# Kernel optimization log

Measured on AMD Instinct MI355X. Metric: run time of the kernel, lower is better.

## Reference

```python
import jax, jax.numpy as jnp
import numpy as np

B, T, D, H, W = 2, 16, 64, 64, 64
E, EXP = 4, 2
TWO_D = 2 * D
HID = EXP * TWO_D


def layernorm(x, g, b, eps=1e-5):
    m = x.mean(-1, keepdims=True)
    v = ((x - m) ** 2).mean(-1, keepdims=True)
    return (x - m) / jnp.sqrt(v + eps) * g + b


def pscan(A, X):
    # h_t = A_t * h_{t-1} + X_t, scanned over axis=1 (time); complex-valued.
    def comb(c1, c2):
        a1, x1 = c1
        a2, x2 = c2
        return a1 * a2, a2 * x1 + x2
    return jax.lax.associative_scan(comb, (A, X), axis=1)[1]


def setup_inputs() -> dict:
    key = jax.random.key(0)
    ks = jax.random.split(key, 24)
    def s(i, shape, scale=0.05):
        return jax.random.normal(ks[i], shape, jnp.float32) * scale
    return {
        "x_re": jax.random.normal(ks[0], (B, T, D, H, W), jnp.float32),
        "x_im": jax.random.normal(ks[1], (B, T, D, H, W), jnp.float32),
        "dt": jax.random.uniform(ks[2], (T,), jnp.float32, 0.5, 1.5),
        "ln_s_g": jnp.ones((TWO_D,), jnp.float32),
        "ln_s_b": jnp.zeros((TWO_D,), jnp.float32),
        "conv_w": s(3, (TWO_D, TWO_D, 3, 3)),
        "conv_b": jnp.zeros((TWO_D,), jnp.float32),
        "ln_t_g": jnp.ones((TWO_D,), jnp.float32),
        "ln_t_b": jnp.zeros((TWO_D,), jnp.float32),
        "enc_re": s(4, (D, D)), "enc_im": s(5, (D, D)),
        "dec_re": s(6, (D, D)), "dec_im": s(7, (D, D)),
        "alpha": s(8, (D,), 0.5), "omega": s(9, (D,), 1.0),
        "wg": s(10, (TWO_D, D)), "bg": jnp.zeros((D,), jnp.float32),
        "p_re": s(11, (D, D)), "p_im": s(12, (D, D)),
        "w_drift": s(13, (TWO_D, D)), "b_drift": jnp.zeros((D,), jnp.float32),
        "w_router": s(14, (TWO_D, E)),
        "w1": s(15, (E, TWO_D, HID)), "w2": s(16, (E, HID, TWO_D)),
        "noise_scale": jnp.float32(0.01),
    }


def reference(x_re, x_im, dt, ln_s_g, ln_s_b, conv_w, conv_b, ln_t_g, ln_t_b,
              enc_re, enc_im, dec_re, dec_im, alpha, omega, wg, bg,
              p_re, p_im, w_drift, b_drift, w_router, w1, w2, noise_scale):
    x = x_re + 1j * x_im  # [B,T,D,H,W] complex64
    N = B * T
    xf = x.reshape(N, D, H, W)
    xr = jnp.concatenate([xf.real, xf.imag], axis=1)  # [N,2D,H,W]
    # spatial LayerNorm over channels
    xn = layernorm(xr.transpose(0, 2, 3, 1), ln_s_g, ln_s_b).transpose(0, 3, 1, 2)
    # Clifford spatial conv (standard 3x3 same-conv on stacked re/im channels)
    xs = jax.lax.conv_general_dilated(xn, conv_w, (1, 1), 'SAME',
                                      dimension_numbers=('NCHW', 'OIHW', 'NCHW'))
    xs = xs + conv_b[None, :, None, None]
    x_sc = xs[:, :D] + 1j * xs[:, D:]            # [N,D,H,W]
    x5 = x_sc.reshape(B, T, D, H, W)              # complex
    # basis encode: complex channel mixing
    enc = enc_re + 1j * enc_im
    u_t = jnp.einsum('bthwd,de->bthwe', x5.transpose(0, 1, 3, 4, 2), enc)  # [B,T,H,W,D]

    # ---- global flux tracker (pscan #1) ----
    x_mean = x5.mean(axis=(-2, -1))               # [B,T,D] complex
    feat = jnp.concatenate([x_mean.real, x_mean.imag], axis=-1)  # [B,T,2D]
    gate = jax.nn.sigmoid(feat @ wg + bg)         # [B,T,D]
    flux_A = gate.astype(jnp.complex64)
    flux_X = (1.0 - gate) * x_mean
    flux_state = pscan(flux_A, flux_X)            # [B,T,D]
    flux_out = flux_state @ (p_re + 1j * p_im)    # [B,T,D]
    drift_in = jnp.concatenate([flux_out.real, flux_out.imag], axis=-1)
    drift = drift_in @ w_drift + b_drift          # [B,T,D] (dead code in source; kept for fidelity)
    drift_c = drift[..., : D // 2] + 1j * drift[..., D // 2:]
    del drift_c

    # ---- temporal propagation (pscan #2) ----
    dt_e = dt.reshape(1, T, 1, 1, 1)              # broadcast (B,T,H,W,1)
    lam = -jax.nn.softplus(alpha) + 1j * omega    # [D]
    decay = jnp.exp(lam * dt_e)                   # [1,T,1,1,D]
    forcing = (decay - 1.0) / lam                 # ZOH forcing operator
    u_scaled = u_t * forcing                      # [B,T,H,W,D]
    decay_full = jnp.broadcast_to(decay, (B, T, H, W, D))
    A_time = decay_full.transpose(0, 2, 3, 1, 4).reshape(B * H * W, T, D)
    X_time = u_scaled.transpose(0, 2, 3, 1, 4).reshape(B * H * W, T, D)
    Y = pscan(A_time, X_time)
    u_out = Y.reshape(B, H, W, T, D).transpose(0, 3, 1, 2, 4)  # [B,T,H,W,D]
    # deterministic surrogate for the SDE stochastic term (state-proportional)
    u_out = u_out + noise_scale * jnp.sqrt(dt_e) * u_out
    dec = dec_re + 1j * dec_im
    x_out = jnp.einsum('bthwd,de->bthwe', u_out, dec)  # decode
    x_out = x_out.transpose(0, 1, 4, 2, 3).reshape(N, D, H, W)
    xo_r = jnp.concatenate([x_out.real, x_out.imag], axis=1)
    xo_n = layernorm(xo_r.transpose(0, 2, 3, 1), ln_t_g, ln_t_b)  # [N,H,W,2D]

    # ---- MoE FFN over pixels (soft mixture of experts) ----
    gates = jax.nn.softmax(xo_n @ w_router, axis=-1)  # [N,H,W,E]
    acc = jnp.zeros_like(xo_n)
    for e in range(E):
        h = jax.nn.gelu(xo_n @ w1[e])
        acc = acc + gates[..., e:e + 1] * (h @ w2[e])
    delta = acc[..., :D] + 1j * acc[..., D:]          # [N,H,W,D]
    delta = delta.transpose(0, 3, 1, 2).reshape(B, T, D, H, W)
    return x + delta
```

## Files before the change

### kernel.cpp

```cpp
#include <hip/hip_runtime.h>
#include <hip/hip_bf16.h>

#define BB 2
#define TT 16
#define DD 64
#define HH 64
#define WW 64
#define NPIX 131072


typedef unsigned short u16;
typedef unsigned int u32;
typedef __attribute__((ext_vector_type(8))) short bf16x8;
typedef __attribute__((ext_vector_type(4))) float f32x4;

union U16x8 { uint4 u4; uint2 u2[2]; u16 h[8]; bf16x8 v; };

__device__ __forceinline__ float us2f(u16 u) {
  union { u32 i; float f; } c; c.i = ((u32)u) << 16; return c.f;
}
__device__ __forceinline__ u16 f2us(float f) {
  u32 x = __float_as_uint(f);
  u32 r = x + 0x7fffu + ((x >> 16) & 1u);
  return (u16)(r >> 16);
}

__global__ __launch_bounds__(256) void k0_prep(
    const float* __restrict__ conv_w,
    const float* __restrict__ enc_re, const float* __restrict__ enc_im,
    const float* __restrict__ dec_re, const float* __restrict__ dec_im,
    const float* __restrict__ w1, const float* __restrict__ w2,
    u16* __restrict__ mencs, u16* __restrict__ mdecs,
    u16* __restrict__ wcs, u16* __restrict__ w1s, u16* __restrict__ w2s) {
  int idx = blockIdx.x * 256 + threadIdx.x;
  if (idx < 65536) {
    int m = idx >> 15;
    int z = idx & 32767;
    int s = z >> 14;
    int q = z & 16383;
    int j = q & 7, lane = (q >> 3) & 63, ks = (q >> 9) & 3, nt = (q >> 11) & 7;
    int k = ks * 32 + (lane >> 4) * 8 + j;
    int n = nt * 16 + (lane & 15);
    const float* mre = m ? dec_re : enc_re;
    const float* mim = m ? dec_im : enc_im;
    float v;
    if (k < 64) v = (n < 64) ?  mre[k * 64 + n]        : mim[k * 64 + n - 64];
    else        v = (n < 64) ? -mim[(k - 64) * 64 + n] : mre[(k - 64) * 64 + n - 64];
    u16 hi = f2us(v);
    u16 val = s ? f2us(v - us2f(hi)) : hi;
    u16* dst = m ? mdecs : mencs;
    dst[((nt * 8 + s * 4 + ks) * 64 + lane) * 8 + j] = val;
  } else if (idx < 212992) {
    int z = idx - 65536;
    int j = z & 7, lane = (z >> 3) & 63, ks = (z >> 9) & 3, nt = (z >> 11) & 7, tap = z >> 14;
    int ic = ks * 32 + (lane >> 4) * 8 + j;
    int oc = nt * 16 + (lane & 15);
    wcs[z] = f2us(conv_w[(oc * 128 + ic) * 9 + tap]);
  } else if (idx < 344064) {
    int z = idx - 212992;
    int j = z & 7, lane = (z >> 3) & 63, ks = (z >> 9) & 3, nt = (z >> 11) & 15, e = z >> 15;
    int k = ks * 32 + (lane >> 4) * 8 + j;
    int nn = nt * 16 + (lane & 15);
    w1s[z] = f2us(w1[e * 32768 + k * 256 + nn]);
  } else if (idx < 475136) {
    int z = idx - 344064;
    int j = z & 7, lane = (z >> 3) & 63, ks = (z >> 9) & 7, nt = (z >> 12) & 7, e = z >> 15;
    int k = ks * 32 + (lane >> 4) * 8 + j;
    int nn = nt * 16 + (lane & 15);
    w2s[z] = f2us(w2[e * 32768 + k * 128 + nn]);
  }
}

__global__ __launch_bounds__(256) void k1_spatial_ln(
    const float* __restrict__ x_re, const float* __restrict__ x_im,
    const float* __restrict__ g, const float* __restrict__ b,
    u16* __restrict__ xn) {
  __shared__ float tile[64 * 129];
  __shared__ float meanA[64], rstdA[64];
  int n = blockIdx.x >> 6, h = blockIdx.x & 63;
  int tid = threadIdx.x;
  for (int k = 0; k < 32; ++k) {
    int flat = tid + k * 256;
    int c = flat >> 6, w = flat & 63;
    float v = (c < 64) ? x_re[n * 262144 + c * 4096 + h * 64 + w]
                       : x_im[n * 262144 + (c - 64) * 4096 + h * 64 + w];
    tile[w * 129 + c] = v;
  }
  __syncthreads();
  int p = tid >> 2, q = tid & 3;
  float s = 0.f, ss = 0.f;
  for (int c = q * 32; c < q * 32 + 32; ++c) {
    float v = tile[p * 129 + c];
    s += v; ss += v * v;
  }
  s += __shfl_xor(s, 1); ss += __shfl_xor(ss, 1);
  s += __shfl_xor(s, 2); ss += __shfl_xor(ss, 2);
  if (q == 0) {
    float m = s * (1.0f / 128.0f);
    float var = ss * (1.0f / 128.0f) - m * m;
    meanA[p] = m; rstdA[p] = rsqrtf(var + 1e-5f);
  }
  __syncthreads();
  int rowbase = (n * 4096 + h * 64) * 128;
  for (int k = 0; k < 32; ++k) {
    int flat = tid + k * 256;
    int pp = flat >> 7, c = flat & 127;
    float v = (tile[pp * 129 + c] - meanA[pp]) * rstdA[pp] * g[c] + b[c];
    xn[rowbase + flat] = f2us(v);
  }
}

__global__ __launch_bounds__(256) void k2_mfma(
    const u16* __restrict__ xn, const u16* __restrict__ wcs,
    const float* __restrict__ conv_b, u16* __restrict__ xs) {
  __shared__ __align__(16) u16 Xs[3 * 66 * 132];
  int tid = threadIdx.x;
  int wave = tid >> 6, lane = tid & 63;
  int quad = lane >> 4, am = lane & 15;
  int n = blockIdx.x >> 6, h = blockIdx.x & 63;

  for (int dh = 0; dh < 3; ++dh) {
    int hs = h + dh - 1;
    bool valid = (hs >= 0) && (hs < 64);
    const u16* src = xn + (n * 4096 + hs * 64) * 128;
    for (int c = 0; c < 4; ++c) {
      int f8 = tid + c * 256;
      int px = f8 >> 4, ch = (f8 & 15) * 8;
      uint2 lo = make_uint2(0, 0), hi = make_uint2(0, 0);
      if (valid) {
        const uint2* s2 = (const uint2*)(src + px * 128 + ch);
        lo = s2[0]; hi = s2[1];
      }
      u16* dst = Xs + (dh * 66 + px + 1) * 132 + ch;
      *(uint2*)dst = lo;
      *(uint2*)(dst + 4) = hi;
    }
  }
  for (int z = tid; z < 792; z += 256) {
    int dh = z / 264, r = z % 264;
    int px = (r < 132) ? 0 : 65;
    Xs[(dh * 66 + px) * 132 + (r % 132)] = 0;
  }
  __syncthreads();

  f32x4 acc[8];
#pragma unroll
  for (int nt = 0; nt < 8; ++nt) {
    float bv = conv_b[nt * 16 + am];
    acc[nt] = (f32x4){bv, bv, bv, bv};
  }
  int mt = wave;
  for (int tap = 0; tap < 9; ++tap) {
    int dh = tap / 3, dw = tap % 3;
    const u16* arow = Xs + (dh * 66 + mt * 16 + am + dw) * 132 + quad * 8;
    bf16x8 a[4];
#pragma unroll
    for (int ks = 0; ks < 4; ++ks) {
      U16x8 t;
      t.u2[0] = *(const uint2*)(arow + ks * 32);
      t.u2[1] = *(const uint2*)(arow + ks * 32 + 4);
      a[ks] = t.v;
    }
    const uint4* wp = (const uint4*)wcs + tap * 2048 + lane;
    uint4 wb[4];
#pragma unroll
    for (int ks = 0; ks < 4; ++ks) wb[ks] = wp[ks * 64];
    for (int nt = 0; nt < 8; ++nt) {
      uint4 wn[4];
      if (nt < 7) {
#pragma unroll
        for (int ks = 0; ks < 4; ++ks) wn[ks] = wp[((nt + 1) * 4 + ks) * 64];
      }
#pragma unroll
      for (int ks = 0; ks < 4; ++ks) {
        U16x8 bf; bf.u4 = wb[ks];
        acc[nt] = __builtin_amdgcn_mfma_f32_16x16x32_bf16(a[ks], bf.v, acc[nt], 0, 0, 0);
      }
      if (nt < 7) {
#pragma unroll
        for (int ks = 0; ks < 4; ++ks) wb[ks] = wn[ks];
      }
    }
  }
  int rowg = n * 4096 + h * 64;
#pragma unroll
  for (int nt = 0; nt < 8; ++nt)
#pragma unroll
    for (int r = 0; r < 4; ++r)
      xs[(rowg + mt * 16 + quad * 4 + r) * 128 + nt * 16 + am] = f2us(acc[nt][r]);
}

__global__ __launch_bounds__(256) void k3_mfma(
    u16* X, const u16* __restrict__ ms) {
  int tid = threadIdx.x;
  int wave = tid >> 6, lane = tid & 63;
  int quad = lane >> 4, am = lane & 15;
  int rowbase = blockIdx.x * 128 + wave * 32;

  bf16x8 ax[2][4];
#pragma unroll
  for (int mt = 0; mt < 2; ++mt) {
    const uint4* ar = (const uint4*)(X + (rowbase + mt * 16 + am) * 128 + quad * 8);
#pragma unroll
    for (int ks = 0; ks < 4; ++ks) { U16x8 t; t.u4 = ar[ks * 4]; ax[mt][ks] = t.v; }
  }
  const uint4* mp = (const uint4*)ms + lane;
  uint4 wb[8];
#pragma unroll
  for (int kk = 0; kk < 8; ++kk) wb[kk] = mp[kk * 64];
  for (int nt = 0; nt < 8; ++nt) {
    uint4 wn[8];
    if (nt < 7) {
#pragma unroll
      for (int kk = 0; kk < 8; ++kk) wn[kk] = mp[((nt + 1) * 8 + kk) * 64];
    }
    f32x4 ca = (f32x4){0.f, 0.f, 0.f, 0.f};
    f32x4 cb = (f32x4){0.f, 0.f, 0.f, 0.f};
#pragma unroll
    for (int kk = 0; kk < 8; ++kk) {
      U16x8 bf; bf.u4 = wb[kk];
      ca = __builtin_amdgcn_mfma_f32_16x16x32_bf16(ax[0][kk & 3], bf.v, ca, 0, 0, 0);
      cb = __builtin_amdgcn_mfma_f32_16x16x32_bf16(ax[1][kk & 3], bf.v, cb, 0, 0, 0);
    }
#pragma unroll
    for (int r = 0; r < 4; ++r) {
      X[(rowbase + quad * 4 + r) * 128 + nt * 16 + am]      = f2us(ca[r]);
      X[(rowbase + 16 + quad * 4 + r) * 128 + nt * 16 + am] = f2us(cb[r]);
    }
    if (nt < 7) {
#pragma unroll
      for (int kk = 0; kk < 8; ++kk) wb[kk] = wn[kk];
    }
  }
}

__global__ __launch_bounds__(256) void k_scan(
    u16* __restrict__ u, const float* __restrict__ dt,
    const float* __restrict__ alpha, const float* __restrict__ omega,
    const float* __restrict__ ns_p) {
  int flat = blockIdx.x * 256 + threadIdx.x;
  int d = flat & 63;
  int hw = (flat >> 6) & 4095;
  int b = flat >> 18;
  float a = alpha[d];
  float sp = (a > 20.f) ? a : log1pf(expf(a));
  float lr = -sp, li = omega[d];
  float inv_l2 = 1.0f / (lr * lr + li * li);
  float ns = ns_p[0];
  float yr = 0.f, yi = 0.f;
  const int stride = 4096 * 128;
  int base0 = b * 16 * stride + hw * 128 + d;
  for (int t = 0; t < 16; ++t) {
    float dtv = dt[t];
    float er = expf(lr * dtv);
    float ang = li * dtv;
    float dr = er * cosf(ang), di = er * sinf(ang);
    float fr = ((dr - 1.f) * lr + di * li) * inv_l2;
    float fi = (di * lr - (dr - 1.f) * li) * inv_l2;
    int idx = base0 + t * stride;
    float ur = us2f(u[idx]), ui = us2f(u[idx + 64]);
    float usr = ur * fr - ui * fi;
    float usi = ur * fi + ui * fr;
    float nyr = dr * yr - di * yi + usr;
    float nyi = dr * yi + di * yr + usi;
    yr = nyr; yi = nyi;
    float sc = 1.0f + ns * sqrtf(dtv);
    u[idx] = f2us(yr * sc);
    u[idx + 64] = f2us(yi * sc);
  }
}

__global__ __launch_bounds__(256) void k4_mfma(
    const u16* __restrict__ U, const u16* __restrict__ ms,
    const float* __restrict__ g, const float* __restrict__ bb,
    u16* __restrict__ xo) {
  int tid = threadIdx.x;
  int wave = tid >> 6, lane = tid & 63;
  int quad = lane >> 4, am = lane & 15;
  int rowbase = blockIdx.x * 128 + wave * 32;

  bf16x8 ax[2][4];
#pragma unroll
  for (int mt = 0; mt < 2; ++mt) {
    const uint4* ar = (const uint4*)(U + (rowbase + mt * 16 + am) * 128 + quad * 8);
#pragma unroll
    for (int ks = 0; ks < 4; ++ks) { U16x8 t; t.u4 = ar[ks * 4]; ax[mt][ks] = t.v; }
  }
  float gv[8], bv[8];
#pragma unroll
  for (int nt = 0; nt < 8; ++nt) { gv[nt] = g[nt * 16 + am]; bv[nt] = bb[nt * 16 + am]; }

  const uint4* mp = (const uint4*)ms + lane;
  f32x4 acc[2][8];
#pragma unroll
  for (int mt = 0; mt < 2; ++mt)
#pragma unroll
    for (int nt = 0; nt < 8; ++nt) acc[mt][nt] = (f32x4){0.f, 0.f, 0.f, 0.f};

  uint4 wb[8];
#pragma unroll
  for (int kk = 0; kk < 8; ++kk) wb[kk] = mp[kk * 64];
  for (int nt = 0; nt < 8; ++nt) {
    uint4 wn[8];
    if (nt < 7) {
#pragma unroll
      for (int kk = 0; kk < 8; ++kk) wn[kk] = mp[((nt + 1) * 8 + kk) * 64];
    }
#pragma unroll
    for (int kk = 0; kk < 8; ++kk) {
      U16x8 bf; bf.u4 = wb[kk];
      acc[0][nt] = __builtin_amdgcn_mfma_f32_16x16x32_bf16(ax[0][kk & 3], bf.v, acc[0][nt], 0, 0, 0);
      acc[1][nt] = __builtin_amdgcn_mfma_f32_16x16x32_bf16(ax[1][kk & 3], bf.v, acc[1][nt], 0, 0, 0);
    }
    if (nt < 7) {
#pragma unroll
      for (int kk = 0; kk < 8; ++kk) wb[kk] = wn[kk];
    }
  }

#pragma unroll
  for (int mt = 0; mt < 2; ++mt) {
#pragma unroll
    for (int r = 0; r < 4; ++r) {
      float s = 0.f, ss = 0.f;
#pragma unroll
      for (int nt = 0; nt < 8; ++nt) { float v = acc[mt][nt][r]; s += v; ss += v * v; }
      s += __shfl_xor(s, 1); ss += __shfl_xor(ss, 1);
      s += __shfl_xor(s, 2); ss += __shfl_xor(ss, 2);
      s += __shfl_xor(s, 4); ss += __shfl_xor(ss, 4);
      s += __shfl_xor(s, 8); ss += __shfl_xor(ss, 8);
      float m = s * (1.0f / 128.0f);
      float var = ss * (1.0f / 128.0f) - m * m;
      float rstd = rsqrtf(var + 1e-5f);
      u16* xop = xo + (rowbase + mt * 16 + quad * 4 + r) * 128 + am;
#pragma unroll
      for (int nt = 0; nt < 8; ++nt)
        xop[nt * 16] = f2us((acc[mt][nt][r] - m) * rstd * gv[nt] + bv[nt]);
    }
  }
}

__global__ __launch_bounds__(256) void k5_mfma(
    const u16* __restrict__ xo, const u16* __restrict__ w1s,
    const u16* __restrict__ w2s, const float* __restrict__ w_router,
    const float* __restrict__ x_re, const float* __restrict__ x_im,
    u16* __restrict__ out) {
  __shared__ __align__(16) u16 Hs[128 * 276];
  __shared__ float gate_s[128 * 4];
  int tid = threadIdx.x;
  int wave = tid >> 6, lane = tid & 63;
  int quad = lane >> 4, am = lane & 15;
  int rowbase = blockIdx.x * 128 + wave * 32;

  for (int pp = 0; pp < 2; ++pp) {
    int pxl = wave * 32 + pp * 16 + am;
    const uint4* xr = (const uint4*)(xo + (blockIdx.x * 128 + pxl) * 128);
    float acc = 0.f;
    for (int c8 = 0; c8 < 16; ++c8) {
      U16x8 t; t.u4 = xr[c8];
#pragma unroll
      for (int j = 0; j < 8; ++j)
        acc += us2f(t.h[j]) * w_router[(c8 * 8 + j) * 4 + quad];
    }
    float mx = fmaxf(acc, __shfl_xor(acc, 16));
    mx = fmaxf(mx, __shfl_xor(mx, 32));
    float ex = __expf(acc - mx);
    float sm = ex + __shfl_xor(ex, 16);
    sm += __shfl_xor(sm, 32);
    gate_s[pxl * 4 + quad] = ex / sm;
  }

  bf16x8 ax[2][4];
#pragma unroll
  for (int mt = 0; mt < 2; ++mt) {
    const uint4* ar = (const uint4*)(xo + (rowbase + mt * 16 + am) * 128 + quad * 8);
#pragma unroll
    for (int ks = 0; ks < 4; ++ks) { U16x8 t; t.u4 = ar[ks * 4]; ax[mt][ks] = t.v; }
  }

  f32x4 c2[2][8];
#pragma unroll
  for (int mt = 0; mt < 2; ++mt)
#pragma unroll
    for (int nt = 0; nt < 8; ++nt) c2[mt][nt] = (f32x4){0.f, 0.f, 0.f, 0.f};

  for (int e = 0; e < 4; ++e) {
    const uint4* w1p = (const uint4*)w1s + e * 4096 + lane;
    uint4 wb[4];
#pragma unroll
    for (int ks = 0; ks < 4; ++ks) wb[ks] = w1p[ks * 64];
    for (int nt = 0; nt < 16; ++nt) {
      uint4 wn[4];
      if (nt < 15) {
#pragma unroll
        for (int ks = 0; ks < 4; ++ks) wn[ks] = w1p[((nt + 1) * 4 + ks) * 64];
      }
      f32x4 c1a = (f32x4){0.f, 0.f, 0.f, 0.f};
      f32x4 c1b = (f32x4){0.f, 0.f, 0.f, 0.f};
#pragma unroll
      for (int ks = 0; ks < 4; ++ks) {
        U16x8 bf; bf.u4 = wb[ks];
        c1a = __builtin_amdgcn_mfma_f32_16x16x32_bf16(ax[0][ks], bf.v, c1a, 0, 0, 0);
        c1b = __builtin_amdgcn_mfma_f32_16x16x32_bf16(ax[1][ks], bf.v, c1b, 0, 0, 0);
      }
#pragma unroll
      for (int r = 0; r < 4; ++r) {
        float v = c1a[r];
        float t = 0.7978845608f * (v + 0.044715f * v * v * v);
        float sg = 1.0f - __builtin_amdgcn_rcpf(1.0f + __expf(2.0f * t));
        float g0 = gate_s[(wave * 32 + quad * 4 + r) * 4 + e];
        Hs[(wave * 32 + quad * 4 + r) * 276 + nt * 16 + am] = f2us(v * sg * g0);
        v = c1b[r];
        t = 0.7978845608f * (v + 0.044715f * v * v * v);
        sg = 1.0f - __builtin_amdgcn_rcpf(1.0f + __expf(2.0f * t));
        float g1 = gate_s[(wave * 32 + 16 + quad * 4 + r) * 4 + e];
        Hs[(wave * 32 + 16 + quad * 4 + r) * 276 + nt * 16 + am] = f2us(v * sg * g1);
      }
      if (nt < 15) {
#pragma unroll
        for (int ks = 0; ks < 4; ++ks) wb[ks] = wn[ks];
      }
    }
    const uint4* w2p = (const uint4*)w2s + e * 4096 + lane;
    uint4 wb2[8];
#pragma unroll
    for (int nt = 0; nt < 8; ++nt) wb2[nt] = w2p[(nt * 8) * 64];
    for (int ks = 0; ks < 8; ++ks) {
      uint4 wn2[8];
      if (ks < 7) {
#pragma unroll
        for (int nt = 0; nt < 8; ++nt) wn2[nt] = w2p[(nt * 8 + ks + 1) * 64];
      }
      U16x8 a2[2];
#pragma unroll
      for (int mt = 0; mt < 2; ++mt) {
        const u16* hr = Hs + (wave * 32 + mt * 16 + am) * 276 + ks * 32 + quad * 8;
        a2[mt].u2[0] = *(const uint2*)hr;
        a2[mt].u2[1] = *(const uint2*)(hr + 4);
      }
#pragma unroll
      for (int nt = 0; nt < 8; ++nt) {
        U16x8 bf; bf.u4 = wb2[nt];
        c2[0][nt] = __builtin_amdgcn_mfma_f32_16x16x32_bf16(a2[0].v, bf.v, c2[0][nt], 0, 0, 0);
        c2[1][nt] = __builtin_amdgcn_mfma_f32_16x16x32_bf16(a2[1].v, bf.v, c2[1][nt], 0, 0, 0);
      }
      if (ks < 7) {
#pragma unroll
        for (int nt = 0; nt < 8; ++nt) wb2[nt] = wn2[nt];
      }
    }
  }

  __syncthreads();
  float* Os = (float*)Hs;
#pragma unroll
  for (int nt = 0; nt < 4; ++nt)
#pragma unroll
    for (int mt = 0; mt < 2; ++mt)
#pragma unroll
      for (int r = 0; r < 4; ++r) {
        int pxl = wave * 32 + mt * 16 + quad * 4 + r;
        Os[(nt * 16 + am) * 129 + pxl]      = c2[mt][nt][r];
        Os[(64 + nt * 16 + am) * 129 + pxl] = c2[mt][nt + 4][r];
      }
  __syncthreads();
  int nb  = (blockIdx.x * 128) >> 12;
  int hw0 = (blockIdx.x * 128) & 4095;
#pragma unroll
  for (int k = 0; k < 32; ++k) {
    int flat = tid + k * 256;
    int d = flat >> 7, px = flat & 127;
    int gidx = (nb * 64 + d) * 4096 + hw0 + px;
    float rr = x_re[gidx] + Os[d * 129 + px];
    float ii = x_im[gidx] + Os[(64 + d) * 129 + px];
    ((u32*)out)[gidx] = (u32)f2us(ii) | ((u32)f2us(rr) << 16);
  }
}

extern "C" void kernel_launch(void* const* d_in, const int* in_sizes, int n_in,
                              void* d_out, int out_size, void* d_ws, size_t ws_size,
                              hipStream_t stream) {
  const float* x_re     = (const float*)d_in[0];
  const float* x_im     = (const float*)d_in[1];
  const float* dt       = (const float*)d_in[2];
  const float* ln_s_g   = (const float*)d_in[3];
  const float* ln_s_b   = (const float*)d_in[4];
  const float* conv_w   = (const float*)d_in[5];
  const float* conv_b   = (const float*)d_in[6];
  const float* ln_t_g   = (const float*)d_in[7];
  const float* ln_t_b   = (const float*)d_in[8];
  const float* enc_re   = (const float*)d_in[9];
  const float* enc_im   = (const float*)d_in[10];
  const float* dec_re   = (const float*)d_in[11];
  const float* dec_im   = (const float*)d_in[12];
  const float* alpha    = (const float*)d_in[13];
  const float* omega    = (const float*)d_in[14];
  const float* w_router = (const float*)d_in[21];
  const float* w1       = (const float*)d_in[22];
  const float* w2       = (const float*)d_in[23];
  const float* ns       = (const float*)d_in[24];

  u16*   buf   = (u16*)d_ws;
  u16*   mencs = (u16*)((char*)d_ws + 33554432);
  u16*   mdecs = mencs + 32768;
  u16*   wcs   = mdecs + 32768;
  u16*   w1s   = wcs + 147456;
  u16*   w2s   = w1s + 131072;
  u16*   outf  = (u16*)d_out;

  k0_prep<<<1856, 256, 0, stream>>>(conv_w, enc_re, enc_im, dec_re, dec_im,
                                    w1, w2, mencs, mdecs, wcs, w1s, w2s);
  k1_spatial_ln<<<2048, 256, 0, stream>>>(x_re, x_im, ln_s_g, ln_s_b, buf);
  k2_mfma<<<2048, 256, 0, stream>>>(buf, wcs, conv_b, outf);
  k3_mfma<<<1024, 256, 0, stream>>>(outf, mencs);
  k_scan<<<2048, 256, 0, stream>>>(outf, dt, alpha, omega, ns);
  k4_mfma<<<1024, 256, 0, stream>>>(outf, mdecs, ln_t_g, ln_t_b, buf);
  k5_mfma<<<1024, 256, 0, stream>>>(buf, w1s, w2s, w_router, x_re, x_im, outf);
}
```

Measured before the change: 465.3 us.

## Halve MoE hidden LDS buffer by splitting expert FFN into two hidden halves

Splits each expert's 256-wide hidden layer into two 128-wide halves, running W1 then W2 for each half, so the shared-memory hidden buffer shrinks from 128x276 to 128x140 bf16. The output transpose staging is also split into two 32-channel passes so it fits in the smaller buffer. The GELU expression is algebraically simplified to fold the gate multiply and drop one multiply. Less LDS per block is meant to let more blocks run per CU, at the cost of extra barriers and two passes through the epilogue.

```diff
diff --git a/kernel.cpp b/kernel.cpp
--- a/kernel.cpp
+++ b/kernel.cpp
@@ -345,7 +345,7 @@
     const u16* __restrict__ w2s, const float* __restrict__ w_router,
     const float* __restrict__ x_re, const float* __restrict__ x_im,
     u16* __restrict__ out) {
-  __shared__ __align__(16) u16 Hs[128 * 276];
+  __shared__ __align__(16) u16 Hs[128 * 140];
   __shared__ float gate_s[128 * 4];
   int tid = threadIdx.x;
   int wave = tid >> 6, lane = tid & 63;
@@ -384,96 +384,103 @@
 #pragma unroll
     for (int nt = 0; nt < 8; ++nt) c2[mt][nt] = (f32x4){0.f, 0.f, 0.f, 0.f};
 
+  const float GA = 1.5957691216f, GB = 0.07135481283f;
+
   for (int e = 0; e < 4; ++e) {
-    const uint4* w1p = (const uint4*)w1s + e * 4096 + lane;
-    uint4 wb[4];
-#pragma unroll
-    for (int ks = 0; ks < 4; ++ks) wb[ks] = w1p[ks * 64];
-    for (int nt = 0; nt < 16; ++nt) {
-      uint4 wn[4];
-      if (nt < 15) {
-#pragma unroll
-        for (int ks = 0; ks < 4; ++ks) wn[ks] = w1p[((nt + 1) * 4 + ks) * 64];
+    for (int hh = 0; hh < 2; ++hh) {
+      const uint4* w1p = (const uint4*)w1s + e * 4096 + hh * 2048 + lane;
+      uint4 wb[4];
+#pragma unroll
+      for (int ks = 0; ks < 4; ++ks) wb[ks] = w1p[ks * 64];
+      for (int ntl = 0; ntl < 8; ++ntl) {
+        uint4 wn[4];
+        if (ntl < 7) {
+#pragma unroll
+          for (int ks = 0; ks < 4; ++ks) wn[ks] = w1p[((ntl + 1) * 4 + ks) * 64];
+        }
+        f32x4 c1a = (f32x4){0.f, 0.f, 0.f, 0.f};
+        f32x4 c1b = (f32x4){0.f, 0.f, 0.f, 0.f};
+#pragma unroll
+        for (int ks = 0; ks < 4; ++ks) {
+          U16x8 bf; bf.u4 = wb[ks];
+          c1a = __builtin_amdgcn_mfma_f32_16x16x32_bf16(ax[0][ks], bf.v, c1a, 0, 0, 0);
+          c1b = __builtin_amdgcn_mfma_f32_16x16x32_bf16(ax[1][ks], bf.v, c1b, 0, 0, 0);
+        }
+#pragma unroll
+        for (int r = 0; r < 4; ++r) {
+          float v = c1a[r];
+          float gv0 = gate_s[(wave * 32 + quad * 4 + r) * 4 + e] * v;
+          float t2 = v * (GA + GB * v * v);
+          float rc = __builtin_amdgcn_rcpf(1.0f + __expf(t2));
+          Hs[(wave * 32 + quad * 4 + r) * 140 + ntl * 16 + am] = f2us(gv0 - gv0 * rc);
+          v = c1b[r];
+          float gv1 = gate_s[(wave * 32 + 16 + quad * 4 + r) * 4 + e] * v;
+          t2 = v * (GA + GB * v * v);
+          rc = __builtin_amdgcn_rcpf(1.0f + __expf(t2));
+          Hs[(wave * 32 + 16 + quad * 4 + r) * 140 + ntl * 16 + am] = f2us(gv1 - gv1 * rc);
+        }
+        if (ntl < 7) {
+#pragma unroll
+          for (int ks = 0; ks < 4; ++ks) wb[ks] = wn[ks];
+        }
       }
-      f32x4 c1a = (f32x4){0.f, 0.f, 0.f, 0.f};
-      f32x4 c1b = (f32x4){0.f, 0.f, 0.f, 0.f};
-#pragma unroll
-      for (int ks = 0; ks < 4; ++ks) {
-        U16x8 bf; bf.u4 = wb[ks];
-        c1a = __builtin_amdgcn_mfma_f32_16x16x32_bf16(ax[0][ks], bf.v, c1a, 0, 0, 0);
-        c1b = __builtin_amdgcn_mfma_f32_16x16x32_bf16(ax[1][ks], bf.v, c1b, 0, 0, 0);
+      const uint4* w2p = (const uint4*)w2s + e * 4096 + lane;
+      uint4 wb2[8];
+#pragma unroll
+      for (int nt = 0; nt < 8; ++nt) wb2[nt] = w2p[(nt * 8 + hh * 4) * 64];
+      for (int ksl = 0; ksl < 4; ++ksl) {
+        uint4 wn2[8];
+        if (ksl < 3) {
+#pragma unroll
+          for (int nt = 0; nt < 8; ++nt) wn2[nt] = w2p[(nt * 8 + hh * 4 + ksl + 1) * 64];
+        }
+        U16x8 a2[2];
+#pragma unroll
+        for (int mt = 0; mt < 2; ++mt) {
+          const u16* hr = Hs + (wave * 32 + mt * 16 + am) * 140 + ksl * 32 + quad * 8;
+          a2[mt].u2[0] = *(const uint2*)hr;
+          a2[mt].u2[1] = *(const uint2*)(hr + 4);
+        }
+#pragma unroll
+        for (int nt = 0; nt < 8; ++nt) {
+          U16x8 bf; bf.u4 = wb2[nt];
+          c2[0][nt] = __builtin_amdgcn_mfma_f32_16x16x32_bf16(a2[0].v, bf.v, c2[0][nt], 0, 0, 0);
+          c2[1][nt] = __builtin_amdgcn_mfma_f32_16x16x32_bf16(a2[1].v, bf.v, c2[1][nt], 0, 0, 0);
+        }
+        if (ksl < 3) {
+#pragma unroll
+          for (int nt = 0; nt < 8; ++nt) wb2[nt] = wn2[nt];
+        }
       }
-#pragma unroll
-      for (int r = 0; r < 4; ++r) {
-        float v = c1a[r];
-        float t = 0.7978845608f * (v + 0.044715f * v * v * v);
-        float sg = 1.0f - __builtin_amdgcn_rcpf(1.0f + __expf(2.0f * t));
-        float g0 = gate_s[(wave * 32 + quad * 4 + r) * 4 + e];
-        Hs[(wave * 32 + quad * 4 + r) * 276 + nt * 16 + am] = f2us(v * sg * g0);
-        v = c1b[r];
-        t = 0.7978845608f * (v + 0.044715f * v * v * v);
-        sg = 1.0f - __builtin_amdgcn_rcpf(1.0f + __expf(2.0f * t));
-        float g1 = gate_s[(wave * 32 + 16 + quad * 4 + r) * 4 + e];
-        Hs[(wave * 32 + 16 + quad * 4 + r) * 276 + nt * 16 + am] = f2us(v * sg * g1);
-      }
-      if (nt < 15) {
-#pragma unroll
-        for (int ks = 0; ks < 4; ++ks) wb[ks] = wn[ks];
-      }
-    }
-    const uint4* w2p = (const uint4*)w2s + e * 4096 + lane;
-    uint4 wb2[8];
-#pragma unroll
-    for (int nt = 0; nt < 8; ++nt) wb2[nt] = w2p[(nt * 8) * 64];
-    for (int ks = 0; ks < 8; ++ks) {
-      uint4 wn2[8];
-      if (ks < 7) {
-#pragma unroll
-        for (int nt = 0; nt < 8; ++nt) wn2[nt] = w2p[(nt * 8 + ks + 1) * 64];
-      }
-      U16x8 a2[2];
-#pragma unroll
-      for (int mt = 0; mt < 2; ++mt) {
-        const u16* hr = Hs + (wave * 32 + mt * 16 + am) * 276 + ks * 32 + quad * 8;
-        a2[mt].u2[0] = *(const uint2*)hr;
-        a2[mt].u2[1] = *(const uint2*)(hr + 4);
-      }
-#pragma unroll
-      for (int nt = 0; nt < 8; ++nt) {
-        U16x8 bf; bf.u4 = wb2[nt];
-        c2[0][nt] = __builtin_amdgcn_mfma_f32_16x16x32_bf16(a2[0].v, bf.v, c2[0][nt], 0, 0, 0);
-        c2[1][nt] = __builtin_amdgcn_mfma_f32_16x16x32_bf16(a2[1].v, bf.v, c2[1][nt], 0, 0, 0);
-      }
-      if (ks < 7) {
-#pragma unroll
-        for (int nt = 0; nt < 8; ++nt) wb2[nt] = wn2[nt];
-      }
-    }
-  }
-
-  __syncthreads();
+    }
+  }
+
   float* Os = (float*)Hs;
-#pragma unroll
-  for (int nt = 0; nt < 4; ++nt)
-#pragma unroll
-    for (int mt = 0; mt < 2; ++mt)
-#pragma unroll
-      for (int r = 0; r < 4; ++r) {
-        int pxl = wave * 32 + mt * 16 + quad * 4 + r;
-        Os[(nt * 16 + am) * 129 + pxl]      = c2[mt][nt][r];
-        Os[(64 + nt * 16 + am) * 129 + pxl] = c2[mt][nt + 4][r];
-      }
-  __syncthreads();
   int nb  = (blockIdx.x * 128) >> 12;
   int hw0 = (blockIdx.x * 128) & 4095;
 #pragma unroll
-  for (int k = 0; k < 32; ++k) {
-    int flat = tid + k * 256;
-    int d = flat >> 7, px = flat & 127;
-    int gidx = (nb * 64 + d) * 4096 + hw0 + px;
-    float rr = x_re[gidx] + Os[d * 129 + px];
-    float ii = x_im[gidx] + Os[(64 + d) * 129 + px];
-    ((u32*)out)[gidx] = (u32)f2us(ii) | ((u32)f2us(rr) << 16);
+  for (int p = 0; p < 2; ++p) {
+    __syncthreads();
+#pragma unroll
+    for (int nt2 = 0; nt2 < 2; ++nt2)
+#pragma unroll
+      for (int mt = 0; mt < 2; ++mt)
+#pragma unroll
+        for (int r = 0; r < 4; ++r) {
+          int pxl = wave * 32 + mt * 16 + quad * 4 + r;
+          Os[(nt2 * 16 + am) * 129 + pxl]        = c2[mt][2 * p + nt2][r];
+          Os[(32 + nt2 * 16 + am) * 129 + pxl]   = c2[mt][4 + 2 * p + nt2][r];
+        }
+    __syncthreads();
+#pragma unroll
+    for (int k = 0; k < 16; ++k) {
+      int flat = tid + k * 256;
+      int dl = flat >> 7, px = flat & 127;
+      int gidx = (nb * 64 + p * 32 + dl) * 4096 + hw0 + px;
+      float rr = x_re[gidx] + Os[dl * 129 + px];
+      float ii = x_im[gidx] + Os[(32 + dl) * 129 + px];
+      ((u32*)out)[gidx] = (u32)f2us(ii) | ((u32)f2us(rr) << 16);
+    }
   }
 }
 
```

After: 492.3 us. 1.06x slower.
